# Kernel tuning notes

Hardware: AMD Instinct MI355X
Metric: run time of the kernel (lower is better)

Reference implementation:

```python
import jax, jax.numpy as jnp
import numpy as np

B, N, DIM = 16, 3136, 512
HEADS, AGENT, WINDOW = 8, 49, 14


def setup_inputs() -> dict:
    key = jax.random.key(0)
    ks = jax.random.split(key, 14)
    s = 0.02
    return {
        "x": jax.random.normal(ks[0], (B, N, DIM), jnp.float32),
        "w_qkv": jax.random.normal(ks[1], (3 * DIM, DIM), jnp.float32) * 0.02,
        "w_proj": jax.random.normal(ks[2], (DIM, DIM), jnp.float32) * 0.02,
        "b_proj": jnp.zeros((DIM,), jnp.float32),
        "w_dwc": jax.random.normal(ks[3], (DIM, 1, 3, 3), jnp.float32) * 0.1,
        "b_dwc": jnp.zeros((DIM,), jnp.float32),
        "an_bias": jax.random.normal(ks[4], (HEADS, AGENT, 7, 7), jnp.float32) * s,
        "na_bias": jax.random.normal(ks[5], (HEADS, AGENT, 7, 7), jnp.float32) * s,
        "ah_bias": jax.random.normal(ks[6], (1, HEADS, AGENT, WINDOW, 1), jnp.float32) * s,
        "aw_bias": jax.random.normal(ks[7], (1, HEADS, AGENT, 1, WINDOW), jnp.float32) * s,
        "ha_bias": jax.random.normal(ks[8], (1, HEADS, WINDOW, 1, AGENT), jnp.float32) * s,
        "wa_bias": jax.random.normal(ks[9], (1, HEADS, 1, WINDOW, AGENT), jnp.float32) * s,
        "ca_bias": jax.random.normal(ks[10], (1, HEADS, 1, AGENT), jnp.float32) * s,
    }


def reference(x, w_qkv, w_proj, b_proj, w_dwc, b_dwc, an_bias, na_bias,
              ah_bias, aw_bias, ha_bias, wa_bias, ca_bias):
    b, n, c = x.shape
    h = w = int(np.sqrt(n))            # 56x56, static
    nh, hd = HEADS, c // HEADS
    scale = hd ** -0.5
    ww = WINDOW * WINDOW               # 196

    qkv = x @ w_qkv.T                  # (b, n, 3c)
    q, k, v = jnp.split(qkv, 3, axis=-1)

    # agent tokens: adaptive avg-pool q to (7, 7)  (exact block mean, 56/7=8)
    pool = int(AGENT ** 0.5)
    q_img = q.reshape(b, h, w, c).transpose(0, 3, 1, 2)  # (b, c, h, w)
    pooled = q_img.reshape(b, c, pool, h // pool, pool, w // pool).mean(axis=(3, 5))
    agent = pooled.reshape(b, c, AGENT).transpose(0, 2, 1)  # (b, 49, c)

    qh = q.reshape(b, n, nh, hd).transpose(0, 2, 1, 3)      # (b, H, n, d)
    kh = k.reshape(b, n, nh, hd).transpose(0, 2, 1, 3)
    vh = v.reshape(b, n, nh, hd).transpose(0, 2, 1, 3)
    ah = agent.reshape(b, AGENT, nh, hd).transpose(0, 2, 1, 3)  # (b, H, 49, d)

    # ---- stage 1: agent -> kv attention ----
    pb1 = jax.image.resize(an_bias, (nh, AGENT, WINDOW, WINDOW), 'bilinear')
    pb1 = pb1.reshape(1, nh, AGENT, ww)
    pb2 = (ah_bias + aw_bias).reshape(1, nh, AGENT, ww)
    pb = jnp.broadcast_to(pb1 + pb2, (b, nh, AGENT, ww))
    scores1 = jnp.einsum('bhad,bhnd->bhan', ah * scale, kh)     # (b, H, 49, n)
    pb_up = jax.image.resize(pb, scores1.shape, 'bilinear')     # 196 -> n along last dim
    attn1 = jax.nn.softmax(scores1 + pb_up, axis=-1)
    agent_v = jnp.einsum('bhan,bhnd->bhad', attn1, vh)          # (b, H, 49, d)

    # ---- stage 2: query -> agent attention ----
    ab1 = jax.image.resize(na_bias, (nh, AGENT, WINDOW, WINDOW), 'bilinear')
    ab1 = ab1.reshape(1, nh, AGENT, ww).transpose(0, 1, 3, 2)   # (1, H, 196, 49)
    ab2 = (ha_bias + wa_bias).reshape(1, nh, ww, AGENT)
    ab = jnp.broadcast_to(ab1 + ab2, (b, nh, ww, AGENT))
    ab = jnp.concatenate([jnp.broadcast_to(ca_bias, (b, nh, 1, AGENT)), ab], axis=-2)
    scores2 = jnp.einsum('bhnd,bhad->bhna', qh * scale, ah)     # (b, H, n, 49)
    ab_up = jax.image.resize(ab, scores2.shape, 'bilinear')     # 197 -> n along dim -2
    attn2 = jax.nn.softmax(scores2 + ab_up, axis=-1)
    out = jnp.einsum('bhna,bhad->bhnd', attn2, agent_v)
    out = out.transpose(0, 2, 1, 3).reshape(b, n, c)

    # ---- depthwise-conv residual on v ----
    v_img = vh.transpose(0, 2, 1, 3).reshape(b, h, w, c).transpose(0, 3, 1, 2)
    dwc = jax.lax.conv_general_dilated(
        v_img, w_dwc, (1, 1), 'SAME',
        dimension_numbers=('NCHW', 'OIHW', 'NCHW'), feature_group_count=c)
    dwc = dwc + b_dwc[None, :, None, None]
    out = out + dwc.transpose(0, 2, 3, 1).reshape(b, n, c)

    return out @ w_proj.T + b_proj
```

## Files before the change

kernel.cpp:

```cpp
#include <hip/hip_runtime.h>

typedef unsigned short u16;
typedef unsigned int   u32;
typedef unsigned long long u64;
typedef float  f32x4  __attribute__((ext_vector_type(4)));
typedef __bf16 bf16x8 __attribute__((ext_vector_type(8)));

#define DEV static __device__ __forceinline__

DEV float bf2f(u16 u){ union{float f;u32 i;}v; v.i=((u32)u)<<16; return v.f; }
DEV float bflo(u32 u){ union{float f;u32 i;}v; v.i=u<<16; return v.f; }
DEV float bfhi(u32 u){ union{float f;u32 i;}v; v.i=u&0xffff0000u; return v.f; }
DEV u16   f2bf(float f){ union{float f;u32 i;}v; v.f=f; return (u16)((v.i + 0x7fffu + ((v.i>>16)&1u))>>16); }

DEV void async16(const void* g, void* l){
  __builtin_amdgcn_global_load_lds((const __attribute__((address_space(1))) void*)g,
                                   (__attribute__((address_space(3))) void*)l, 16, 0, 0);
}

__global__ __launch_bounds__(256) void cast_bf16(const float* __restrict__ in,
                                                 u16* __restrict__ out, int n4)
{
  int i = blockIdx.x*256 + threadIdx.x;
  if (i >= n4) return;
  float4 v = ((const float4*)in)[i];
  ushort4 o;
  o.x = f2bf(v.x); o.y = f2bf(v.y); o.z = f2bf(v.z); o.w = f2bf(v.w);
  ((ushort4*)out)[i] = o;
}

__global__ __launch_bounds__(512, 2) void gemm256(
    const u16* __restrict__ A, const u16* __restrict__ W, int K, int mode,
    u16* __restrict__ oq, u16* __restrict__ okk, u16* __restrict__ ov,
    float* __restrict__ of, const float* __restrict__ bias)
{
  __shared__ __align__(16) u16 As[2*16384];
  __shared__ __align__(16) u16 Bs[2*16384];
  const int tid  = threadIdx.x;
  const int w = tid >> 6, lane = tid & 63;
  const int wm = w >> 2, wn = w & 3;
  const int r16 = lane & 15, q4 = lane >> 4;
  const int xr = r16 & 7;

  const int ny  = gridDim.y;
  const int nwg = (int)gridDim.x * ny;
  const int cpx = nwg >> 3;
  const int hw  = blockIdx.x + gridDim.x*blockIdx.y;
  const int lb  = (hw & 7)*cpx + (hw >> 3);
  const int tx  = lb / ny;
  const int ty  = lb - tx*ny;

  const size_t Abase = (size_t)tx * 256 * K;
  const size_t Bbase = (size_t)ty * 256 * K;
  const int NT = K >> 6;

#define STAGE(t, half, arr) do { \
    const u16* _src = (arr) ? (W + Bbase) : (A + Abase); \
    u16* _dst = ((arr) ? Bs : As) + (((t) & 1) * 16384 + (half) * 8192); \
    const int _k0 = (t) << 6; \
    _Pragma("unroll") \
    for (int _i = 0; _i < 2; _i++) { \
      int _s = _i*512 + tid; \
      int _row = _s >> 3; \
      int _c = (_s & 7) ^ (_row & 7); \
      async16(_src + (size_t)((half)*128 + _row) * K + _k0 + _c*8, (char*)_dst + (size_t)_s * 16); \
    } \
  } while(0)

#define READ_A(MI0) do { \
    _Pragma("unroll") \
    for (int _i = 0; _i < 4; _i++) { \
      int _row = wm*128 + ((MI0)+_i)*16 + r16; \
      _Pragma("unroll") \
      for (int _ks = 0; _ks < 2; _ks++) \
        af[_i][_ks] = *(const bf16x8*)&As[boff + _row*64 + (((_ks*4 + q4) ^ xr) * 8)]; \
    } \
  } while(0)

#define READ_B() do { \
    _Pragma("unroll") \
    for (int _j = 0; _j < 4; _j++) { \
      int _row = wn*64 + _j*16 + r16; \
      _Pragma("unroll") \
      for (int _ks = 0; _ks < 2; _ks++) \
        bfr[_j][_ks] = *(const bf16x8*)&Bs[boff + _row*64 + (((_ks*4 + q4) ^ xr) * 8)]; \
    } \
  } while(0)

#define MFMA_Q(MI0, NI0) do { \
    _Pragma("unroll") \
    for (int _ks = 0; _ks < 2; _ks++) \
      _Pragma("unroll") \
      for (int _i = 0; _i < 4; _i++) \
        _Pragma("unroll") \
        for (int _j = 0; _j < 2; _j++) \
          acc[(MI0)+_i][(NI0)+_j] = __builtin_amdgcn_mfma_f32_16x16x32_bf16( \
              bfr[(NI0)+_j][_ks], af[_i][_ks], acc[(MI0)+_i][(NI0)+_j], 0,0,0); \
  } while(0)

  f32x4 acc[8][4];
  #pragma unroll
  for (int i=0;i<8;i++)
    #pragma unroll
    for (int j=0;j<4;j++) acc[i][j] = (f32x4){0.f,0.f,0.f,0.f};
  bf16x8 af[4][2], bfr[4][2];

  STAGE(0,0,0); STAGE(0,1,0); STAGE(0,0,1); STAGE(0,1,1);
  STAGE(1,0,1); STAGE(1,0,0); STAGE(1,1,0);
  asm volatile("s_waitcnt vmcnt(6)" ::: "memory");
  __builtin_amdgcn_s_barrier();

  for (int T = 0; T < NT; ++T) {
    const int boff = (T & 1) * 16384;
    READ_A(0);
    READ_B();
    if (T+1 < NT) STAGE(T+1, 1, 1);
    __builtin_amdgcn_s_barrier();
    asm volatile("s_waitcnt lgkmcnt(0)" ::: "memory");
    __builtin_amdgcn_sched_barrier(0);
    __builtin_amdgcn_s_setprio(1);
    MFMA_Q(0, 0);
    MFMA_Q(0, 2);
    __builtin_amdgcn_s_setprio(0);
    __builtin_amdgcn_s_barrier();
    READ_A(4);
    if (T+2 < NT) STAGE(T+2, 0, 1);
    __builtin_amdgcn_s_barrier();
    asm volatile("s_waitcnt lgkmcnt(0)" ::: "memory");
    __builtin_amdgcn_sched_barrier(0);
    __builtin_amdgcn_s_setprio(1);
    MFMA_Q(4, 0);
    __builtin_amdgcn_s_setprio(0);
    __builtin_amdgcn_s_barrier();
    if (T+2 < NT) { STAGE(T+2, 0, 0); STAGE(T+2, 1, 0); }
    __builtin_amdgcn_s_setprio(1);
    MFMA_Q(4, 2);
    __builtin_amdgcn_s_setprio(0);
    if (T+2 < NT)      asm volatile("s_waitcnt vmcnt(6)" ::: "memory");
    else if (T+1 < NT) asm volatile("s_waitcnt vmcnt(0)" ::: "memory");
    __builtin_amdgcn_s_barrier();
  }

#undef STAGE
#undef READ_A
#undef READ_B
#undef MFMA_Q

  const int m0  = tx*256 + wm*128;
  const int n0g = ty*256 + wn*64;
  if (mode == 0){
    int sel = ty >> 1;
    u16* dst = sel==0 ? oq : (sel==1 ? okk : ov);
    #pragma unroll
    for (int i=0;i<8;i++){
      int token = m0 + i*16 + r16;
      #pragma unroll
      for (int j=0;j<4;j++){
        int col = (n0g + j*16 + q4*4) & 511;
        uint2 pk;
        pk.x = (u32)f2bf(acc[i][j][0]) | ((u32)f2bf(acc[i][j][1]) << 16);
        pk.y = (u32)f2bf(acc[i][j][2]) | ((u32)f2bf(acc[i][j][3]) << 16);
        *(uint2*)&dst[(size_t)token*512 + col] = pk;
      }
    }
  } else {
    #pragma unroll
    for (int j=0;j<4;j++){
      int nbase = n0g + j*16 + q4*4;
      float4 b4 = *(const float4*)&bias[nbase];
      #pragma unroll
      for (int i=0;i<8;i++){
        int token = m0 + i*16 + r16;
        float4 o4 = { acc[i][j][0]+b4.x, acc[i][j][1]+b4.y,
                      acc[i][j][2]+b4.z, acc[i][j][3]+b4.w };
        *(float4*)&of[(size_t)token*512 + nbase] = o4;
      }
    }
  }
}

__global__ __launch_bounds__(256) void pool_q(const u16* __restrict__ qb, u16* __restrict__ agentb)
{
  int idx = blockIdx.x*256 + threadIdx.x;
  int c8 = idx & 63;
  int ba = idx >> 6;
  int a = ba & 63, b = ba >> 6;
  u16* dst = agentb + ((size_t)(b*64 + a))*512 + c8*8;
  if (a >= 49) { *(uint4*)dst = (uint4){0,0,0,0}; return; }
  int ay = a / 7, ax = a % 7;
  const u16* base = qb + ((size_t)b*3136 + (size_t)(ay*8)*56 + ax*8)*512 + c8*8;
  float acc[8] = {0.f,0.f,0.f,0.f,0.f,0.f,0.f,0.f};
  #pragma unroll
  for (int iy=0; iy<8; iy++){
    #pragma unroll
    for (int ix=0; ix<8; ix++){
      uint4 uv = *(const uint4*)(base + ((size_t)(iy*56 + ix) << 9));
      u32 uu[4] = {uv.x, uv.y, uv.z, uv.w};
      #pragma unroll
      for (int e=0;e<4;e++){ acc[2*e+0] += bflo(uu[e]); acc[2*e+1] += bfhi(uu[e]); }
    }
  }
  uint4 pk;
  pk.x = (u32)f2bf(acc[0]*0.015625f) | ((u32)f2bf(acc[1]*0.015625f) << 16);
  pk.y = (u32)f2bf(acc[2]*0.015625f) | ((u32)f2bf(acc[3]*0.015625f) << 16);
  pk.z = (u32)f2bf(acc[4]*0.015625f) | ((u32)f2bf(acc[5]*0.015625f) << 16);
  pk.w = (u32)f2bf(acc[6]*0.015625f) | ((u32)f2bf(acc[7]*0.015625f) << 16);
  *(uint4*)dst = pk;
}

DEV void lin1(float c, int S, int& i0, int& i1, float& w){
  if (c <= 0.f){ i0=0; i1=0; w=0.f; }
  else if (c >= (float)(S-1)){ i0=S-1; i1=S-1; w=0.f; }
  else { i0=(int)c; i1=i0+1; w=c-(float)i0; }
}
DEV float bilin7(const float* s, int Y, int X){
  int y0,y1,x0,x1; float wy,wx;
  lin1(0.5f*Y - 0.25f, 7, y0,y1,wy);
  lin1(0.5f*X - 0.25f, 7, x0,x1,wx);
  float v0 = s[y0*7+x0] + wx*(s[y0*7+x1]-s[y0*7+x0]);
  float v1 = s[y1*7+x0] + wx*(s[y1*7+x1]-s[y1*7+x0]);
  return v0 + wy*(v1 - v0);
}
__global__ __launch_bounds__(256) void bias_pre(
    const float* __restrict__ an_bias, const float* __restrict__ na_bias,
    const float* __restrict__ ah_bias, const float* __restrict__ aw_bias,
    const float* __restrict__ ha_bias, const float* __restrict__ wa_bias,
    const float* __restrict__ ca_bias, float* __restrict__ PB, float* __restrict__ AB)
{
  int idx = blockIdx.x*256 + threadIdx.x;
  if (idx < 8*49*196){
    int j = idx % 196; int ha = idx / 196; int a = ha % 49, h = ha / 49;
    int wy = j / 14, wx = j % 14;
    PB[idx] = bilin7(an_bias + (h*49+a)*49, wy, wx)
            + ah_bias[(h*49+a)*14 + wy] + aw_bias[(h*49+a)*14 + wx];
  }
  int idx2 = idx - 8*49*196;
  if (idx2 >= 0 && idx2 < 8*197*49){
    int a = idx2 % 49; int hr = idx2 / 49; int r = hr % 197, h = hr / 197;
    float v;
    if (r == 0) v = ca_bias[h*49 + a];
    else {
      int j = r - 1; int wy = j / 14, wx = j % 14;
      v = bilin7(na_bias + (h*49+a)*49, wy, wx)
        + ha_bias[(h*14+wy)*49 + a] + wa_bias[(h*14+wx)*49 + a];
    }
    AB[idx2] = v;
  }
}

__global__ __launch_bounds__(256) void bias_expand2(
    const float* __restrict__ PB, const float* __restrict__ AB,
    float* __restrict__ PBIT, float* __restrict__ ABI)
{
  int idx = blockIdx.x*256 + threadIdx.x;
  if (idx < 1605632) {
    int a = idx & 63; int t = idx >> 6; int n = t % 3136; int h = t / 3136;
    float val = -1e30f;
    if (a < 49) {
      const float* row = PB + (h*49 + a)*196;
      float c1 = (n + 0.5f)*0.0625f - 0.5f;
      if (c1 <= 0.f) val = row[0];
      else if (c1 >= 195.f) val = row[195];
      else { int j0 = (int)c1; float w = c1 - (float)j0; val = row[j0] + w*(row[j0+1]-row[j0]); }
    }
    PBIT[idx] = val;
  } else {
    int idx2 = idx - 1605632;
    if (idx2 >= 1605632) return;
    int a = idx2 & 63; int t = idx2 >> 6; int n = t % 3136; int h = t / 3136;
    float val = -1e30f;
    if (a < 49) {
      float c2 = (n + 0.5f)*(197.0f/3136.0f) - 0.5f;
      int r0; float w;
      if (c2 <= 0.f) { r0 = 0; w = 0.f; }
      else if (c2 >= 196.f) { r0 = 196; w = 0.f; }
      else { r0 = (int)c2; w = c2 - (float)r0; }
      int r1 = (r0 < 196) ? r0 + 1 : 196;
      float v0 = AB[(h*197 + r0)*49 + a];
      float v1 = AB[(h*197 + r1)*49 + a];
      val = v0 + w*(v1 - v0);
    }
    ABI[idx2] = val;
  }
}

__global__ __launch_bounds__(256) void stage1_mfma(
    const u16* __restrict__ kb, const u16* __restrict__ vb,
    const u16* __restrict__ agentb, const float* __restrict__ PBIT,
    float* __restrict__ pav, float* __restrict__ psum)
{
  int bh = blockIdx.x, chunk = blockIdx.y;
  int b = bh >> 3, h = bh & 7;
  int tid = threadIdx.x, lane = tid & 63, w = tid >> 6;
  int r16 = lane & 15, q4 = lane >> 4;
  __shared__ __align__(16) u16 kld[64*64];
  __shared__ __align__(16) u16 vt[64*68];
  __shared__ __align__(16) u16 scb[64*72];

  int agent = w*16 + r16;
  bf16x8 bah[2];
  {
    const u16* ap = agentb + ((size_t)(b*64 + agent))*512 + h*64 + q4*8;
    bah[0] = *(const bf16x8*)ap;
    bah[1] = *(const bf16x8*)(ap + 32);
  }
  f32x4 Oacc[4];
  #pragma unroll
  for (int nt = 0; nt < 4; nt++) Oacc[nt] = (f32x4){0.f,0.f,0.f,0.f};
  float ssum = 0.f;
  int n0 = chunk * 448;
  const u16* kbase = kb + ((size_t)b*3136)*512 + h*64;
  const u16* vbase = vb + ((size_t)b*3136)*512 + h*64;

  for (int it = 0; it < 7; it++) {
    int nt0 = n0 + it*64;
    __syncthreads();
    #pragma unroll
    for (int i = 0; i < 2; i++) {
      int L = w*128 + i*64 + lane;
      int row = L >> 3, colc = (L & 7) ^ (row & 7);
      async16(kbase + (size_t)(nt0 + row)*512 + colc*8, (char*)kld + (w*128 + i*64)*16);
    }
    uint4 va[2]; int vtok[2], vdc[2];
    #pragma unroll
    for (int i = 0; i < 2; i++) {
      int c = tid + i*256;
      vtok[i] = c >> 3; vdc[i] = (c & 7)*8;
      va[i] = *(const uint4*)(vbase + (size_t)(nt0 + vtok[i])*512 + vdc[i]);
    }
    #pragma unroll
    for (int i = 0; i < 2; i++) {
      u32 uu[4] = {va[i].x, va[i].y, va[i].z, va[i].w};
      #pragma unroll
      for (int e = 0; e < 4; e++) {
        vt[(vdc[i] + 2*e + 0)*68 + vtok[i]] = (u16)(uu[e] & 0xffffu);
        vt[(vdc[i] + 2*e + 1)*68 + vtok[i]] = (u16)(uu[e] >> 16);
      }
    }
    __syncthreads();
    f32x4 S[4];
    #pragma unroll
    for (int mt = 0; mt < 4; mt++) S[mt] = (f32x4){0.f,0.f,0.f,0.f};
    #pragma unroll
    for (int ks = 0; ks < 2; ks++)
      #pragma unroll
      for (int mt = 0; mt < 4; mt++) {
        int row = mt*16 + r16;
        int colc = (ks*4 + q4) ^ (row & 7);
        bf16x8 afr = *(const bf16x8*)&kld[row*64 + colc*8];
        S[mt] = __builtin_amdgcn_mfma_f32_16x16x32_bf16(afr, bah[ks], S[mt], 0,0,0);
      }
    #pragma unroll
    for (int mt = 0; mt < 4; mt++) {
      u64 pk = 0;
      #pragma unroll
      for (int r = 0; r < 4; r++) {
        int tokl = mt*16 + q4*4 + r;
        float bias = PBIT[((size_t)h*3136 + nt0 + tokl)*64 + agent];
        float e = __expf(0.125f*S[mt][r] + bias);
        ssum += e;
        pk |= ((u64)f2bf(e)) << (16*r);
      }
      *(u64*)&scb[agent*72 + mt*16 + q4*4] = pk;
    }
    #pragma unroll
    for (int ks = 0; ks < 2; ks++) {
      bf16x8 ap = *(const bf16x8*)&scb[agent*72 + ks*32 + q4*8];
      #pragma unroll
      for (int nt = 0; nt < 4; nt++) {
        union { bf16x8 v; uint2 u[2]; } bb;
        int dim = nt*16 + r16;
        bb.u[0] = *(const uint2*)&vt[dim*68 + ks*32 + q4*8];
        bb.u[1] = *(const uint2*)&vt[dim*68 + ks*32 + q4*8 + 4];
        Oacc[nt] = __builtin_amdgcn_mfma_f32_16x16x32_bf16(ap, bb.v, Oacc[nt], 0,0,0);
      }
    }
  }
  ssum += __shfl_xor(ssum, 16);
  ssum += __shfl_xor(ssum, 32);
  size_t pb = (size_t)chunk*128 + bh;
  #pragma unroll
  for (int nt = 0; nt < 4; nt++)
    #pragma unroll
    for (int r = 0; r < 4; r++)
      pav[(pb*64 + (w*16 + q4*4 + r))*64 + nt*16 + r16] = Oacc[nt][r];
  if (lane < 16) psum[pb*64 + w*16 + lane] = ssum;
}

__global__ __launch_bounds__(256) void reduce_agv(
    const float* __restrict__ pav, const float* __restrict__ psum, u16* __restrict__ avTg)
{
  int idx = blockIdx.x*256 + threadIdx.x;
  int d = idx & 63, a = (idx >> 6) & 63, bh = idx >> 12;
  float val = 0.f;
  if (a < 49) {
    float acc = 0.f, s = 0.f;
    #pragma unroll
    for (int c = 0; c < 7; c++) {
      acc += pav[(((size_t)c*128 + bh)*64 + a)*64 + d];
      s   += psum[((size_t)c*128 + bh)*64 + a];
    }
    val = acc / s;
  }
  avTg[((size_t)bh*64 + d)*72 + a] = f2bf(val);
}

__global__ __launch_bounds__(256) void stage2_mfma(
    const u16* __restrict__ qb, const u16* __restrict__ agentb,
    const u16* __restrict__ avTg, const float* __restrict__ ABI,
    u16* __restrict__ aout)
{
  int bh = blockIdx.x, chunk = blockIdx.y;
  int b = bh >> 3, h = bh & 7;
  int tid = threadIdx.x, lane = tid & 63, w = tid >> 6;
  int r16 = lane & 15, q4 = lane >> 4;
  __shared__ __align__(16) u16 avs[64*72];
  __shared__ __align__(16) u16 scb2[4*16*72];

  const u16* avsrc = avTg + (size_t)bh*4608;
  #pragma unroll
  for (int rr = 0; rr < 3; rr++) {
    int c = rr*256 + w*64 + lane;
    if (c < 576) async16(avsrc + c*8, (char*)avs + ((size_t)rr*256 + w*64)*16);
  }
  bf16x8 bah[4][2];
  #pragma unroll
  for (int nt = 0; nt < 4; nt++) {
    const u16* ap = agentb + ((size_t)(b*64 + nt*16 + r16))*512 + h*64 + q4*8;
    bah[nt][0] = *(const bf16x8*)ap;
    bah[nt][1] = *(const bf16x8*)(ap + 32);
  }
  __syncthreads();

  u16* scw = scb2 + w*16*72;
  for (int t = 0; t < 7; t++) {
    int tok0 = (chunk*28 + w*7 + t)*16;
    bf16x8 aq[2];
    {
      const u16* qp = qb + ((size_t)b*3136 + tok0 + r16)*512 + h*64 + q4*8;
      aq[0] = *(const bf16x8*)qp;
      aq[1] = *(const bf16x8*)(qp + 32);
    }
    f32x4 S[4];
    #pragma unroll
    for (int nt = 0; nt < 4; nt++) S[nt] = (f32x4){0.f,0.f,0.f,0.f};
    #pragma unroll
    for (int ks = 0; ks < 2; ks++)
      #pragma unroll
      for (int nt = 0; nt < 4; nt++)
        S[nt] = __builtin_amdgcn_mfma_f32_16x16x32_bf16(aq[ks], bah[nt][ks], S[nt], 0,0,0);
    float rs[4] = {0.f,0.f,0.f,0.f};
    #pragma unroll
    for (int nt = 0; nt < 4; nt++)
      #pragma unroll
      for (int r = 0; r < 4; r++) {
        int tokl = q4*4 + r;
        float bias = ABI[((size_t)h*3136 + tok0 + tokl)*64 + nt*16 + r16];
        float e = __expf(0.125f*S[nt][r] + bias);
        rs[r] += e;
        scw[tokl*72 + nt*16 + r16] = f2bf(e);
      }
    #pragma unroll
    for (int m = 1; m <= 8; m <<= 1)
      #pragma unroll
      for (int r = 0; r < 4; r++) rs[r] += __shfl_xor(rs[r], m);
    f32x4 O[4];
    #pragma unroll
    for (int nt = 0; nt < 4; nt++) O[nt] = (f32x4){0.f,0.f,0.f,0.f};
    #pragma unroll
    for (int ks = 0; ks < 2; ks++) {
      bf16x8 ap2 = *(const bf16x8*)&scw[r16*72 + ks*32 + q4*8];
      #pragma unroll
      for (int nt = 0; nt < 4; nt++) {
        bf16x8 bv = *(const bf16x8*)&avs[(nt*16 + r16)*72 + ks*32 + q4*8];
        O[nt] = __builtin_amdgcn_mfma_f32_16x16x32_bf16(ap2, bv, O[nt], 0,0,0);
      }
    }
    float inv[4];
    #pragma unroll
    for (int r = 0; r < 4; r++) inv[r] = 1.0f / rs[r];
    #pragma unroll
    for (int nt = 0; nt < 4; nt++)
      #pragma unroll
      for (int r = 0; r < 4; r++)
        aout[((size_t)b*3136 + tok0 + q4*4 + r)*512 + h*64 + nt*16 + r16] = f2bf(O[nt][r]*inv[r]);
  }
}

__global__ __launch_bounds__(256) void dwc_add2(
    const u16* __restrict__ vb, const float* __restrict__ w_dwc,
    const float* __restrict__ b_dwc, u16* __restrict__ io)
{
  int wave = (blockIdx.x << 2) + (threadIdx.x >> 6);
  int lane = threadIdx.x & 63;
  int c0 = lane * 8;

  float wt[9][8];
  {
    float tmp[72];
    const float4* wp = (const float4*)(w_dwc + c0*9);
    #pragma unroll
    for (int i = 0; i < 18; i++) {
      float4 v4 = wp[i];
      tmp[4*i] = v4.x; tmp[4*i+1] = v4.y; tmp[4*i+2] = v4.z; tmp[4*i+3] = v4.w;
    }
    #pragma unroll
    for (int j = 0; j < 8; j++)
      #pragma unroll
      for (int tp = 0; tp < 9; tp++) wt[tp][j] = tmp[j*9 + tp];
  }
  float bias[8];
  {
    const float4* bp = (const float4*)(b_dwc + c0);
    float4 a4 = bp[0], b4 = bp[1];
    bias[0]=a4.x; bias[1]=a4.y; bias[2]=a4.z; bias[3]=a4.w;
    bias[4]=b4.x; bias[5]=b4.y; bias[6]=b4.z; bias[7]=b4.w;
  }

  int t0 = wave * 16;
  int b = t0 / 3136;
  int n0 = t0 - b*3136;
  const u16* vbase = vb + ((size_t)b*3136)*512 + c0;

  for (int ti = 0; ti < 16; ti++) {
    int n = n0 + ti;
    int y = n / 56, x = n - y*56;
    size_t toff = ((size_t)b*3136 + n)*512 + c0;
    float acc[8];
    {
      uint4 uo = *(const uint4*)(io + toff);
      u32 uu[4] = {uo.x, uo.y, uo.z, uo.w};
      #pragma unroll
      for (int e = 0; e < 4; e++) {
        acc[2*e+0] = bflo(uu[e]) + bias[2*e+0];
        acc[2*e+1] = bfhi(uu[e]) + bias[2*e+1];
      }
    }
    #pragma unroll
    for (int dy = 0; dy < 3; dy++) {
      int yy = y + dy - 1;
      if (yy < 0 || yy > 55) continue;
      #pragma unroll
      for (int dx = 0; dx < 3; dx++) {
        int xx = x + dx - 1;
        if (xx < 0 || xx > 55) continue;
        uint4 uv = *(const uint4*)(vbase + ((size_t)(yy*56 + xx) << 9));
        u32 uu[4] = {uv.x, uv.y, uv.z, uv.w};
        const float* wr = wt[dy*3 + dx];
        #pragma unroll
        for (int e = 0; e < 4; e++) {
          acc[2*e+0] += bflo(uu[e]) * wr[2*e+0];
          acc[2*e+1] += bfhi(uu[e]) * wr[2*e+1];
        }
      }
    }
    uint4 pk;
    pk.x = (u32)f2bf(acc[0]) | ((u32)f2bf(acc[1]) << 16);
    pk.y = (u32)f2bf(acc[2]) | ((u32)f2bf(acc[3]) << 16);
    pk.z = (u32)f2bf(acc[4]) | ((u32)f2bf(acc[5]) << 16);
    pk.w = (u32)f2bf(acc[6]) | ((u32)f2bf(acc[7]) << 16);
    *(uint4*)(io + toff) = pk;
  }
}

extern "C" void kernel_launch(void* const* d_in, const int* in_sizes, int n_in,
                              void* d_out, int out_size, void* d_ws, size_t ws_size,
                              hipStream_t stream)
{
  const float* x       = (const float*)d_in[0];
  const float* w_qkv   = (const float*)d_in[1];
  const float* w_proj  = (const float*)d_in[2];
  const float* b_proj  = (const float*)d_in[3];
  const float* w_dwc   = (const float*)d_in[4];
  const float* b_dwc   = (const float*)d_in[5];
  const float* an_bias = (const float*)d_in[6];
  const float* na_bias = (const float*)d_in[7];
  const float* ah_bias = (const float*)d_in[8];
  const float* aw_bias = (const float*)d_in[9];
  const float* ha_bias = (const float*)d_in[10];
  const float* wa_bias = (const float*)d_in[11];
  const float* ca_bias = (const float*)d_in[12];

  if (ws_size < 210000000u) return;

  char* p = (char*)d_ws;
  u16* regA   = (u16*)p;  p += 51380224;
  u16* qb     = (u16*)p;  p += 51380224;
  u16* kb     = (u16*)p;  p += 51380224;
  u16* vb     = (u16*)p;  p += 51380224;
  u16* wqkvb  = (u16*)p;  p += 1572864;
  u16* wprojb = (u16*)p;  p += 524288;
  u16* agentb = (u16*)p;  p += 1048576;
  float* PB   = (float*)p; p += 307456;
  float* AB   = (float*)p; p += 309248;

  float* PBIT = (float*)((char*)regA);
  float* ABI  = (float*)((char*)regA + 6422528);
  float* pav  = (float*)((char*)regA + 12845056);
  float* psum = (float*)((char*)regA + 27525120);
  u16*   avTg = (u16*)  ((char*)regA + 27754496);
  u16*   aout = kb;

  cast_bf16<<<25088, 256, 0, stream>>>(x, regA, 6422528);
  cast_bf16<<<768,   256, 0, stream>>>(w_qkv, wqkvb, 196608);
  cast_bf16<<<256,   256, 0, stream>>>(w_proj, wprojb, 65536);

  gemm256<<<dim3(196,6), 512, 0, stream>>>(regA, wqkvb, 512, 0, qb, kb, vb, nullptr, nullptr);
  pool_q<<<256, 256, 0, stream>>>(qb, agentb);
  bias_pre<<<602, 256, 0, stream>>>(an_bias, na_bias, ah_bias, aw_bias, ha_bias, wa_bias, ca_bias, PB, AB);
  bias_expand2<<<12544, 256, 0, stream>>>(PB, AB, PBIT, ABI);
  stage1_mfma<<<dim3(128,7), 256, 0, stream>>>(kb, vb, agentb, PBIT, pav, psum);
  reduce_agv<<<2048, 256, 0, stream>>>(pav, psum, avTg);
  stage2_mfma<<<dim3(128,7), 256, 0, stream>>>(qb, agentb, avTg, ABI, aout);
  dwc_add2<<<784, 256, 0, stream>>>(vb, w_dwc, b_dwc, aout);
  gemm256<<<dim3(196,2), 512, 0, stream>>>(aout, wprojb, 512, 1, nullptr, nullptr, nullptr,
                                           (float*)d_out, b_proj);
}
```

Before: 526.3 us.

## Process multiple M panels per QKV GEMM block and split B fragment reads

The QKV GEMM now walks two consecutive 256-row M panels per workgroup, halving the grid, so the weight tile pipeline continues across panels without a new launch wave. The epilogue moves inside the K loop and runs each time a panel finishes, then the accumulators are reset. The XCD remap is generalized to handle grid sizes that are not multiples of 8. The B fragment reads are split into two halves to reduce register pressure. The risks are an epilogue stall in the middle of the pipeline and fewer blocks (588) to fill the CUs.

```diff
diff --git a/kernel.cpp b/kernel.cpp
--- a/kernel.cpp
+++ b/kernel.cpp
@@ -30,7 +30,7 @@
 }
 
 __global__ __launch_bounds__(512, 2) void gemm256(
-    const u16* __restrict__ A, const u16* __restrict__ W, int K, int mode,
+    const u16* __restrict__ A, const u16* __restrict__ W, int NPAN, int mode,
     u16* __restrict__ oq, u16* __restrict__ okk, u16* __restrict__ ov,
     float* __restrict__ of, const float* __restrict__ bias)
 {
@@ -44,26 +44,28 @@
 
   const int ny  = gridDim.y;
   const int nwg = (int)gridDim.x * ny;
-  const int cpx = nwg >> 3;
   const int hw  = blockIdx.x + gridDim.x*blockIdx.y;
-  const int lb  = (hw & 7)*cpx + (hw >> 3);
-  const int tx  = lb / ny;
-  const int ty  = lb - tx*ny;
-
-  const size_t Abase = (size_t)tx * 256 * K;
-  const size_t Bbase = (size_t)ty * 256 * K;
-  const int NT = K >> 6;
+  const int q8  = nwg >> 3, r8 = nwg & 7;
+  const int xcd = hw & 7, wi = hw >> 3;
+  const int lb  = (xcd < r8) ? (xcd*(q8+1) + wi) : (r8*(q8+1) + (xcd - r8)*q8 + wi);
+  const int tx0 = (lb / ny) * NPAN;
+  const int ty  = lb - (lb / ny) * ny;
+
+  const size_t Abase = (size_t)tx0 * 256 * 512;
+  const size_t Bbase = (size_t)ty  * 256 * 512;
+  const int NT = NPAN << 3;
 
 #define STAGE(t, half, arr) do { \
-    const u16* _src = (arr) ? (W + Bbase) : (A + Abase); \
+    const u16* _src = (arr) ? (W + Bbase) \
+                            : (A + Abase + ((size_t)((t) >> 3)) * 131072); \
     u16* _dst = ((arr) ? Bs : As) + (((t) & 1) * 16384 + (half) * 8192); \
-    const int _k0 = (t) << 6; \
+    const int _k0 = ((t) & 7) << 6; \
     _Pragma("unroll") \
     for (int _i = 0; _i < 2; _i++) { \
       int _s = _i*512 + tid; \
       int _row = _s >> 3; \
       int _c = (_s & 7) ^ (_row & 7); \
-      async16(_src + (size_t)((half)*128 + _row) * K + _k0 + _c*8, (char*)_dst + (size_t)_s * 16); \
+      async16(_src + (size_t)((half)*128 + _row) * 512 + _k0 + _c*8, (char*)_dst + (size_t)_s * 16); \
     } \
   } while(0)
 
@@ -77,13 +79,13 @@
     } \
   } while(0)
 
-#define READ_B() do { \
+#define READ_B(J0) do { \
     _Pragma("unroll") \
-    for (int _j = 0; _j < 4; _j++) { \
-      int _row = wn*64 + _j*16 + r16; \
+    for (int _j = 0; _j < 2; _j++) { \
+      int _row = wn*64 + ((J0)+_j)*16 + r16; \
       _Pragma("unroll") \
       for (int _ks = 0; _ks < 2; _ks++) \
-        bfr[_j][_ks] = *(const bf16x8*)&Bs[boff + _row*64 + (((_ks*4 + q4) ^ xr) * 8)]; \
+        bfr[(J0)+_j][_ks] = *(const bf16x8*)&Bs[boff + _row*64 + (((_ks*4 + q4) ^ xr) * 8)]; \
     } \
   } while(0)
 
@@ -98,6 +100,12 @@
               bfr[(NI0)+_j][_ks], af[_i][_ks], acc[(MI0)+_i][(NI0)+_j], 0,0,0); \
   } while(0)
 
+#define PH_SYNC() do { \
+    __builtin_amdgcn_s_barrier(); \
+    asm volatile("s_waitcnt lgkmcnt(0)" ::: "memory"); \
+    __builtin_amdgcn_sched_barrier(0); \
+  } while(0)
+
   f32x4 acc[8][4];
   #pragma unroll
   for (int i=0;i<8;i++)
@@ -113,21 +121,22 @@
   for (int T = 0; T < NT; ++T) {
     const int boff = (T & 1) * 16384;
     READ_A(0);
-    READ_B();
+    READ_B(0);
     if (T+1 < NT) STAGE(T+1, 1, 1);
-    __builtin_amdgcn_s_barrier();
-    asm volatile("s_waitcnt lgkmcnt(0)" ::: "memory");
-    __builtin_amdgcn_sched_barrier(0);
+    PH_SYNC();
     __builtin_amdgcn_s_setprio(1);
     MFMA_Q(0, 0);
+    __builtin_amdgcn_s_setprio(0);
+    __builtin_amdgcn_s_barrier();
+    READ_B(2);
+    PH_SYNC();
+    __builtin_amdgcn_s_setprio(1);
     MFMA_Q(0, 2);
     __builtin_amdgcn_s_setprio(0);
     __builtin_amdgcn_s_barrier();
     READ_A(4);
     if (T+2 < NT) STAGE(T+2, 0, 1);
-    __builtin_amdgcn_s_barrier();
-    asm volatile("s_waitcnt lgkmcnt(0)" ::: "memory");
-    __builtin_amdgcn_sched_barrier(0);
+    PH_SYNC();
     __builtin_amdgcn_s_setprio(1);
     MFMA_Q(4, 0);
     __builtin_amdgcn_s_setprio(0);
@@ -139,44 +148,54 @@
     if (T+2 < NT)      asm volatile("s_waitcnt vmcnt(6)" ::: "memory");
     else if (T+1 < NT) asm volatile("s_waitcnt vmcnt(0)" ::: "memory");
     __builtin_amdgcn_s_barrier();
+
+    if ((T & 7) == 7) {
+      const int pan = T >> 3;
+      const int m0  = (tx0 + pan)*256 + wm*128;
+      const int n0g = ty*256 + wn*64;
+      if (mode == 0){
+        int sel = ty >> 1;
+        u16* dst = sel==0 ? oq : (sel==1 ? okk : ov);
+        #pragma unroll
+        for (int i=0;i<8;i++){
+          int token = m0 + i*16 + r16;
+          #pragma unroll
+          for (int j=0;j<4;j++){
+            int col = (n0g + j*16 + q4*4) & 511;
+            uint2 pk;
+            pk.x = (u32)f2bf(acc[i][j][0]) | ((u32)f2bf(acc[i][j][1]) << 16);
+            pk.y = (u32)f2bf(acc[i][j][2]) | ((u32)f2bf(acc[i][j][3]) << 16);
+            *(uint2*)&dst[(size_t)token*512 + col] = pk;
+          }
+        }
+      } else {
+        #pragma unroll
+        for (int j=0;j<4;j++){
+          int nbase = n0g + j*16 + q4*4;
+          float4 b4 = *(const float4*)&bias[nbase];
+          #pragma unroll
+          for (int i=0;i<8;i++){
+            int token = m0 + i*16 + r16;
+            float4 o4 = { acc[i][j][0]+b4.x, acc[i][j][1]+b4.y,
+                          acc[i][j][2]+b4.z, acc[i][j][3]+b4.w };
+            *(float4*)&of[(size_t)token*512 + nbase] = o4;
+          }
+        }
+      }
+      if (T+1 < NT) {
+        #pragma unroll
+        for (int i=0;i<8;i++)
+          #pragma unroll
+          for (int j=0;j<4;j++) acc[i][j] = (f32x4){0.f,0.f,0.f,0.f};
+      }
+    }
   }
 
 #undef STAGE
 #undef READ_A
 #undef READ_B
 #undef MFMA_Q
-
-  const int m0  = tx*256 + wm*128;
-  const int n0g = ty*256 + wn*64;
-  if (mode == 0){
-    int sel = ty >> 1;
-    u16* dst = sel==0 ? oq : (sel==1 ? okk : ov);
-    #pragma unroll
-    for (int i=0;i<8;i++){
-      int token = m0 + i*16 + r16;
-      #pragma unroll
-      for (int j=0;j<4;j++){
-        int col = (n0g + j*16 + q4*4) & 511;
-        uint2 pk;
-        pk.x = (u32)f2bf(acc[i][j][0]) | ((u32)f2bf(acc[i][j][1]) << 16);
-        pk.y = (u32)f2bf(acc[i][j][2]) | ((u32)f2bf(acc[i][j][3]) << 16);
-        *(uint2*)&dst[(size_t)token*512 + col] = pk;
-      }
-    }
-  } else {
-    #pragma unroll
-    for (int j=0;j<4;j++){
-      int nbase = n0g + j*16 + q4*4;
-      float4 b4 = *(const float4*)&bias[nbase];
-      #pragma unroll
-      for (int i=0;i<8;i++){
-        int token = m0 + i*16 + r16;
-        float4 o4 = { acc[i][j][0]+b4.x, acc[i][j][1]+b4.y,
-                      acc[i][j][2]+b4.z, acc[i][j][3]+b4.w };
-        *(float4*)&of[(size_t)token*512 + nbase] = o4;
-      }
-    }
-  }
+#undef PH_SYNC
 }
 
 __global__ __launch_bounds__(256) void pool_q(const u16* __restrict__ qb, u16* __restrict__ agentb)
@@ -605,7 +624,7 @@
   cast_bf16<<<768,   256, 0, stream>>>(w_qkv, wqkvb, 196608);
   cast_bf16<<<256,   256, 0, stream>>>(w_proj, wprojb, 65536);
 
-  gemm256<<<dim3(196,6), 512, 0, stream>>>(regA, wqkvb, 512, 0, qb, kb, vb, nullptr, nullptr);
+  gemm256<<<dim3(98,6), 512, 0, stream>>>(regA, wqkvb, 2, 0, qb, kb, vb, nullptr, nullptr);
   pool_q<<<256, 256, 0, stream>>>(qb, agentb);
   bias_pre<<<602, 256, 0, stream>>>(an_bias, na_bias, ah_bias, aw_bias, ha_bias, wa_bias, ca_bias, PB, AB);
   bias_expand2<<<12544, 256, 0, stream>>>(PB, AB, PBIT, ABI);
@@ -613,6 +632,6 @@
   reduce_agv<<<2048, 256, 0, stream>>>(pav, psum, avTg);
   stage2_mfma<<<dim3(128,7), 256, 0, stream>>>(qb, agentb, avTg, ABI, aout);
   dwc_add2<<<784, 256, 0, stream>>>(vb, w_dwc, b_dwc, aout);
-  gemm256<<<dim3(196,2), 512, 0, stream>>>(aout, wprojb, 512, 1, nullptr, nullptr, nullptr,
+  gemm256<<<dim3(196,2), 512, 0, stream>>>(aout, wprojb, 1, 1, nullptr, nullptr, nullptr,
                                            (float*)d_out, b_proj);
 }
```

Measured after the change: 556.6 us. 5.8% more time.

## Fuse bias interpolation into attention kernels using shared-memory bias slices

Applied to the files above, without the earlier changes.

Removes the bias_expand2 kernel that materialized per-token interpolated bias tables (PBIT, ABI) in global memory. Each stage1/stage2 block now loads the slice of the compact PB/AB tables its token chunk needs into shared memory and does the linear interpolation inline before the exp. This cuts a kernel launch and about 12.8 MB of global writes plus matching reads. In exchange the kernels use more LDS, do extra ALU work per score, and must keep the 32-entry slice window wide enough for each 448-token chunk.

```diff
diff --git a/kernel.cpp b/kernel.cpp
--- a/kernel.cpp
+++ b/kernel.cpp
@@ -248,45 +248,9 @@
   }
 }
 
-__global__ __launch_bounds__(256) void bias_expand2(
-    const float* __restrict__ PB, const float* __restrict__ AB,
-    float* __restrict__ PBIT, float* __restrict__ ABI)
-{
-  int idx = blockIdx.x*256 + threadIdx.x;
-  if (idx < 1605632) {
-    int a = idx & 63; int t = idx >> 6; int n = t % 3136; int h = t / 3136;
-    float val = -1e30f;
-    if (a < 49) {
-      const float* row = PB + (h*49 + a)*196;
-      float c1 = (n + 0.5f)*0.0625f - 0.5f;
-      if (c1 <= 0.f) val = row[0];
-      else if (c1 >= 195.f) val = row[195];
-      else { int j0 = (int)c1; float w = c1 - (float)j0; val = row[j0] + w*(row[j0+1]-row[j0]); }
-    }
-    PBIT[idx] = val;
-  } else {
-    int idx2 = idx - 1605632;
-    if (idx2 >= 1605632) return;
-    int a = idx2 & 63; int t = idx2 >> 6; int n = t % 3136; int h = t / 3136;
-    float val = -1e30f;
-    if (a < 49) {
-      float c2 = (n + 0.5f)*(197.0f/3136.0f) - 0.5f;
-      int r0; float w;
-      if (c2 <= 0.f) { r0 = 0; w = 0.f; }
-      else if (c2 >= 196.f) { r0 = 196; w = 0.f; }
-      else { r0 = (int)c2; w = c2 - (float)r0; }
-      int r1 = (r0 < 196) ? r0 + 1 : 196;
-      float v0 = AB[(h*197 + r0)*49 + a];
-      float v1 = AB[(h*197 + r1)*49 + a];
-      val = v0 + w*(v1 - v0);
-    }
-    ABI[idx2] = val;
-  }
-}
-
 __global__ __launch_bounds__(256) void stage1_mfma(
     const u16* __restrict__ kb, const u16* __restrict__ vb,
-    const u16* __restrict__ agentb, const float* __restrict__ PBIT,
+    const u16* __restrict__ agentb, const float* __restrict__ PB,
     float* __restrict__ pav, float* __restrict__ psum)
 {
   int bh = blockIdx.x, chunk = blockIdx.y;
@@ -296,6 +260,16 @@
   __shared__ __align__(16) u16 kld[64*64];
   __shared__ __align__(16) u16 vt[64*68];
   __shared__ __align__(16) u16 scb[64*72];
+  __shared__ float PBs[64][33];
+
+  int n0 = chunk * 448;
+  int jbase = (int)((n0 + 0.5f)*0.0625f - 0.5f);
+  if (jbase < 0) jbase = 0;
+  for (int i = tid; i < 2048; i += 256) {
+    int a = i >> 5, j = i & 31;
+    int jj = jbase + j; if (jj > 195) jj = 195;
+    PBs[a][j] = (a < 49) ? PB[(h*49 + a)*196 + jj] : 0.f;
+  }
 
   int agent = w*16 + r16;
   bf16x8 bah[2];
@@ -308,7 +282,6 @@
   #pragma unroll
   for (int nt = 0; nt < 4; nt++) Oacc[nt] = (f32x4){0.f,0.f,0.f,0.f};
   float ssum = 0.f;
-  int n0 = chunk * 448;
   const u16* kbase = kb + ((size_t)b*3136)*512 + h*64;
   const u16* vbase = vb + ((size_t)b*3136)*512 + h*64;
 
@@ -356,7 +329,17 @@
       #pragma unroll
       for (int r = 0; r < 4; r++) {
         int tokl = mt*16 + q4*4 + r;
-        float bias = PBIT[((size_t)h*3136 + nt0 + tokl)*64 + agent];
+        int n = nt0 + tokl;
+        float c1 = (n + 0.5f)*0.0625f - 0.5f;
+        float bv;
+        if (c1 <= 0.f) bv = PBs[agent][0];
+        else if (c1 >= 195.f) bv = PBs[agent][195 - jbase];
+        else {
+          int j0 = (int)c1; float ww = c1 - (float)j0;
+          float v0 = PBs[agent][j0 - jbase], v1 = PBs[agent][j0 - jbase + 1];
+          bv = v0 + ww*(v1 - v0);
+        }
+        float bias = (agent < 49) ? bv : -1e30f;
         float e = __expf(0.125f*S[mt][r] + bias);
         ssum += e;
         pk |= ((u64)f2bf(e)) << (16*r);
@@ -407,7 +390,7 @@
 
 __global__ __launch_bounds__(256) void stage2_mfma(
     const u16* __restrict__ qb, const u16* __restrict__ agentb,
-    const u16* __restrict__ avTg, const float* __restrict__ ABI,
+    const u16* __restrict__ avTg, const float* __restrict__ AB,
     u16* __restrict__ aout)
 {
   int bh = blockIdx.x, chunk = blockIdx.y;
@@ -416,6 +399,15 @@
   int r16 = lane & 15, q4 = lane >> 4;
   __shared__ __align__(16) u16 avs[64*72];
   __shared__ __align__(16) u16 scb2[4*16*72];
+  __shared__ float ABs[32][64];
+
+  int rbase = (int)((chunk*448 + 0.5f)*(197.0f/3136.0f) - 0.5f);
+  if (rbase < 0) rbase = 0;
+  for (int i = tid; i < 2048; i += 256) {
+    int j = i >> 6, a = i & 63;
+    int rr = rbase + j; if (rr > 196) rr = 196;
+    ABs[j][a] = (a < 49) ? AB[(h*197 + rr)*49 + a] : 0.f;
+  }
 
   const u16* avsrc = avTg + (size_t)bh*4608;
   #pragma unroll
@@ -455,7 +447,18 @@
       #pragma unroll
       for (int r = 0; r < 4; r++) {
         int tokl = q4*4 + r;
-        float bias = ABI[((size_t)h*3136 + tok0 + tokl)*64 + nt*16 + r16];
+        int n = tok0 + tokl;
+        float c2 = (n + 0.5f)*(197.0f/3136.0f) - 0.5f;
+        int aidx = nt*16 + r16;
+        float bv;
+        if (c2 <= 0.f) bv = ABs[0][aidx];
+        else if (c2 >= 196.f) bv = ABs[196 - rbase][aidx];
+        else {
+          int r0 = (int)c2; float ww = c2 - (float)r0;
+          float v0 = ABs[r0 - rbase][aidx], v1 = ABs[r0 - rbase + 1][aidx];
+          bv = v0 + ww*(v1 - v0);
+        }
+        float bias = (aidx < 49) ? bv : -1e30f;
         float e = __expf(0.125f*S[nt][r] + bias);
         rs[r] += e;
         scw[tokl*72 + nt*16 + r16] = f2bf(e);
@@ -594,8 +597,6 @@
   float* PB   = (float*)p; p += 307456;
   float* AB   = (float*)p; p += 309248;
 
-  float* PBIT = (float*)((char*)regA);
-  float* ABI  = (float*)((char*)regA + 6422528);
   float* pav  = (float*)((char*)regA + 12845056);
   float* psum = (float*)((char*)regA + 27525120);
   u16*   avTg = (u16*)  ((char*)regA + 27754496);
@@ -608,10 +609,9 @@
   gemm256<<<dim3(196,6), 512, 0, stream>>>(regA, wqkvb, 512, 0, qb, kb, vb, nullptr, nullptr);
   pool_q<<<256, 256, 0, stream>>>(qb, agentb);
   bias_pre<<<602, 256, 0, stream>>>(an_bias, na_bias, ah_bias, aw_bias, ha_bias, wa_bias, ca_bias, PB, AB);
-  bias_expand2<<<12544, 256, 0, stream>>>(PB, AB, PBIT, ABI);
-  stage1_mfma<<<dim3(128,7), 256, 0, stream>>>(kb, vb, agentb, PBIT, pav, psum);
+  stage1_mfma<<<dim3(128,7), 256, 0, stream>>>(kb, vb, agentb, PB, pav, psum);
   reduce_agv<<<2048, 256, 0, stream>>>(pav, psum, avTg);
-  stage2_mfma<<<dim3(128,7), 256, 0, stream>>>(qb, agentb, avTg, ABI, aout);
+  stage2_mfma<<<dim3(128,7), 256, 0, stream>>>(qb, agentb, avTg, AB, aout);
   dwc_add2<<<784, 256, 0, stream>>>(vb, w_dwc, b_dwc, aout);
   gemm256<<<dim3(196,2), 512, 0, stream>>>(aout, wprojb, 512, 1, nullptr, nullptr, nullptr,
                                            (float*)d_out, b_proj);
```

After: 544.5 us. +3.4%, slower.

## Process multiple M-panels per GEMM workgroup to reuse the resident W tile

Applied to the files above, without the earlier changes.

The QKV GEMM now has each workgroup loop over NPAN=2 consecutive 256-row panels of A while keeping the same 256-column W slice. The K loop is extended so staging continues across panels without draining the pipeline, and the epilogue is emitted between panels. This halves the grid (98x6) and keeps a continuous software pipeline across panels. The XCD remap is also generalized for grid sizes that are not multiples of 8. The trade-off is fewer workgroups, about 588 for 256 CUs, which worsens tail balance, and an extra epilogue inside the loop.

```diff
diff --git a/kernel.cpp b/kernel.cpp
--- a/kernel.cpp
+++ b/kernel.cpp
@@ -30,7 +30,7 @@
 }
 
 __global__ __launch_bounds__(512, 2) void gemm256(
-    const u16* __restrict__ A, const u16* __restrict__ W, int K, int mode,
+    const u16* __restrict__ A, const u16* __restrict__ W, int NPAN, int mode,
     u16* __restrict__ oq, u16* __restrict__ okk, u16* __restrict__ ov,
     float* __restrict__ of, const float* __restrict__ bias)
 {
@@ -41,23 +41,26 @@
   const int wm = w >> 2, wn = w & 3;
   const int r16 = lane & 15, q4 = lane >> 4;
   const int xr = r16 & 7;
+  const int K = 512;
 
   const int ny  = gridDim.y;
   const int nwg = (int)gridDim.x * ny;
-  const int cpx = nwg >> 3;
   const int hw  = blockIdx.x + gridDim.x*blockIdx.y;
-  const int lb  = (hw & 7)*cpx + (hw >> 3);
-  const int tx  = lb / ny;
-  const int ty  = lb - tx*ny;
-
-  const size_t Abase = (size_t)tx * 256 * K;
-  const size_t Bbase = (size_t)ty * 256 * K;
-  const int NT = K >> 6;
+  const int q8  = nwg >> 3, r8 = nwg & 7;
+  const int xcd = hw & 7, wi = hw >> 3;
+  const int lb  = (xcd < r8) ? (xcd*(q8+1) + wi) : (r8*(q8+1) + (xcd - r8)*q8 + wi);
+  const int tx0 = (lb / ny) * NPAN;
+  const int ty  = lb - (lb / ny) * ny;
+
+  const size_t Abase = (size_t)tx0 * 256 * K;
+  const size_t Bbase = (size_t)ty  * 256 * K;
+  const int NT = NPAN << 3;
 
 #define STAGE(t, half, arr) do { \
-    const u16* _src = (arr) ? (W + Bbase) : (A + Abase); \
+    const u16* _src = (arr) ? (W + Bbase) \
+                            : (A + Abase + ((size_t)((t) >> 3)) * (256*512)); \
     u16* _dst = ((arr) ? Bs : As) + (((t) & 1) * 16384 + (half) * 8192); \
-    const int _k0 = (t) << 6; \
+    const int _k0 = ((t) & 7) << 6; \
     _Pragma("unroll") \
     for (int _i = 0; _i < 2; _i++) { \
       int _s = _i*512 + tid; \
@@ -96,6 +99,40 @@
         for (int _j = 0; _j < 2; _j++) \
           acc[(MI0)+_i][(NI0)+_j] = __builtin_amdgcn_mfma_f32_16x16x32_bf16( \
               bfr[(NI0)+_j][_ks], af[_i][_ks], acc[(MI0)+_i][(NI0)+_j], 0,0,0); \
+  } while(0)
+
+#define EPILOGUE(pan) do { \
+    const int m0  = (tx0 + (pan))*256 + wm*128; \
+    const int n0g = ty*256 + wn*64; \
+    if (mode == 0){ \
+      int sel = ty >> 1; \
+      u16* dst = sel==0 ? oq : (sel==1 ? okk : ov); \
+      _Pragma("unroll") \
+      for (int i=0;i<8;i++){ \
+        int token = m0 + i*16 + r16; \
+        _Pragma("unroll") \
+        for (int j=0;j<4;j++){ \
+          int col = (n0g + j*16 + q4*4) & 511; \
+          uint2 pk; \
+          pk.x = (u32)f2bf(acc[i][j][0]) | ((u32)f2bf(acc[i][j][1]) << 16); \
+          pk.y = (u32)f2bf(acc[i][j][2]) | ((u32)f2bf(acc[i][j][3]) << 16); \
+          *(uint2*)&dst[(size_t)token*512 + col] = pk; \
+        } \
+      } \
+    } else { \
+      _Pragma("unroll") \
+      for (int j=0;j<4;j++){ \
+        int nbase = n0g + j*16 + q4*4; \
+        float4 b4 = *(const float4*)&bias[nbase]; \
+        _Pragma("unroll") \
+        for (int i=0;i<8;i++){ \
+          int token = m0 + i*16 + r16; \
+          float4 o4 = { acc[i][j][0]+b4.x, acc[i][j][1]+b4.y, \
+                        acc[i][j][2]+b4.z, acc[i][j][3]+b4.w }; \
+          *(float4*)&of[(size_t)token*512 + nbase] = o4; \
+        } \
+      } \
+    } \
   } while(0)
 
   f32x4 acc[8][4];
@@ -139,44 +176,23 @@
     if (T+2 < NT)      asm volatile("s_waitcnt vmcnt(6)" ::: "memory");
     else if (T+1 < NT) asm volatile("s_waitcnt vmcnt(0)" ::: "memory");
     __builtin_amdgcn_s_barrier();
-  }
+
+    if ((T & 7) == 7 && T+1 < NT) {
+      EPILOGUE(T >> 3);
+      #pragma unroll
+      for (int i=0;i<8;i++)
+        #pragma unroll
+        for (int j=0;j<4;j++) acc[i][j] = (f32x4){0.f,0.f,0.f,0.f};
+    }
+  }
+
+  EPILOGUE(NPAN - 1);
 
 #undef STAGE
 #undef READ_A
 #undef READ_B
 #undef MFMA_Q
-
-  const int m0  = tx*256 + wm*128;
-  const int n0g = ty*256 + wn*64;
-  if (mode == 0){
-    int sel = ty >> 1;
-    u16* dst = sel==0 ? oq : (sel==1 ? okk : ov);
-    #pragma unroll
-    for (int i=0;i<8;i++){
-      int token = m0 + i*16 + r16;
-      #pragma unroll
-      for (int j=0;j<4;j++){
-        int col = (n0g + j*16 + q4*4) & 511;
-        uint2 pk;
-        pk.x = (u32)f2bf(acc[i][j][0]) | ((u32)f2bf(acc[i][j][1]) << 16);
-        pk.y = (u32)f2bf(acc[i][j][2]) | ((u32)f2bf(acc[i][j][3]) << 16);
-        *(uint2*)&dst[(size_t)token*512 + col] = pk;
-      }
-    }
-  } else {
-    #pragma unroll
-    for (int j=0;j<4;j++){
-      int nbase = n0g + j*16 + q4*4;
-      float4 b4 = *(const float4*)&bias[nbase];
-      #pragma unroll
-      for (int i=0;i<8;i++){
-        int token = m0 + i*16 + r16;
-        float4 o4 = { acc[i][j][0]+b4.x, acc[i][j][1]+b4.y,
-                      acc[i][j][2]+b4.z, acc[i][j][3]+b4.w };
-        *(float4*)&of[(size_t)token*512 + nbase] = o4;
-      }
-    }
-  }
+#undef EPILOGUE
 }
 
 __global__ __launch_bounds__(256) void pool_q(const u16* __restrict__ qb, u16* __restrict__ agentb)
@@ -605,7 +621,7 @@
   cast_bf16<<<768,   256, 0, stream>>>(w_qkv, wqkvb, 196608);
   cast_bf16<<<256,   256, 0, stream>>>(w_proj, wprojb, 65536);
 
-  gemm256<<<dim3(196,6), 512, 0, stream>>>(regA, wqkvb, 512, 0, qb, kb, vb, nullptr, nullptr);
+  gemm256<<<dim3(98,6), 512, 0, stream>>>(regA, wqkvb, 2, 0, qb, kb, vb, nullptr, nullptr);
   pool_q<<<256, 256, 0, stream>>>(qb, agentb);
   bias_pre<<<602, 256, 0, stream>>>(an_bias, na_bias, ah_bias, aw_bias, ha_bias, wa_bias, ca_bias, PB, AB);
   bias_expand2<<<12544, 256, 0, stream>>>(PB, AB, PBIT, ABI);
@@ -613,6 +629,6 @@
   reduce_agv<<<2048, 256, 0, stream>>>(pav, psum, avTg);
   stage2_mfma<<<dim3(128,7), 256, 0, stream>>>(qb, agentb, avTg, ABI, aout);
   dwc_add2<<<784, 256, 0, stream>>>(vb, w_dwc, b_dwc, aout);
-  gemm256<<<dim3(196,2), 512, 0, stream>>>(aout, wprojb, 512, 1, nullptr, nullptr, nullptr,
+  gemm256<<<dim3(196,2), 512, 0, stream>>>(aout, wprojb, 1, 1, nullptr, nullptr, nullptr,
                                            (float*)d_out, b_proj);
 }
```

Measured after the change: 550.8 us. +4.7%, slower.
